# Optimization experiments

Hardware: AMD Instinct MI355X
Metric: run time of the kernel (lower is better)

Reference implementation:

```python
import jax, jax.numpy as jnp
import numpy as np
import math

DIM = 768
HEADS = 12
HEAD_DIM = DIM // HEADS
EPS = 1e-6


def rms_norm(x, w):
    return x * jax.lax.rsqrt(jnp.mean(x * x, axis=-1, keepdims=True) + EPS) * w


def rotate_half(x):
    # torch.cat([-x[..., 1::2], x[..., ::2]], dim=-1)
    return jnp.concatenate([-x[..., 1::2], x[..., ::2]], axis=-1)


def setup_inputs() -> dict:
    key = jax.random.key(0)
    ks = jax.random.split(key, 12)
    b, n = 2, 2048
    s = 0.02
    return {
        "x": jax.random.normal(ks[0], (b, n, DIM), jnp.float32),
        "cos": jax.random.uniform(ks[1], (1, 1, n, HEAD_DIM), jnp.float32),
        "sin": jax.random.uniform(ks[2], (1, 1, n, HEAD_DIM), jnp.float32),
        "mask": jnp.zeros((1, 1, n, n), jnp.float32),
        "wq": jax.random.normal(ks[3], (DIM, DIM), jnp.float32) * s,
        "wk": jax.random.normal(ks[4], (DIM, DIM), jnp.float32) * s,
        "wv": jax.random.normal(ks[5], (DIM, DIM), jnp.float32) * s,
        "wo": jax.random.normal(ks[6], (DIM, DIM), jnp.float32) * s,
        "bo": jnp.zeros((DIM,), jnp.float32),
        "g_attn": jnp.ones((DIM,), jnp.float32),
        "g_ffn": jnp.ones((DIM,), jnp.float32),
        "w1": jax.random.normal(ks[7], (DIM, 4 * DIM), jnp.float32) * s,
        "b1": jnp.zeros((4 * DIM,), jnp.float32),
        "w2": jax.random.normal(ks[8], (4 * DIM, DIM), jnp.float32) * s,
        "b2": jnp.zeros((DIM,), jnp.float32),
    }


def reference(x, cos, sin, mask, wq, wk, wv, wo, bo, g_attn, g_ffn, w1, b1, w2, b2):
    b, n, _ = x.shape
    h = rms_norm(x, g_attn)
    # [b, n, dim] -> [b, heads, n, head_dim]
    def split_heads(t):
        return t.reshape(b, n, HEADS, HEAD_DIM).transpose(0, 2, 1, 3)
    q = split_heads(h @ wq)
    k = split_heads(h @ wk)
    v = split_heads(h @ wv)
    q = q * cos + rotate_half(q) * sin
    k = k * cos + rotate_half(k) * sin
    scores = jnp.einsum("bhqd,bhkd->bhqk", q, k) / math.sqrt(HEAD_DIM)
    scores = scores + mask
    attn = jax.nn.softmax(scores, axis=-1)
    out = jnp.einsum("bhqk,bhkd->bhqd", attn, v)
    out = out.transpose(0, 2, 1, 3).reshape(b, n, DIM)
    x = x + (out @ wo + bo)  # dropout is identity in eval
    h2 = rms_norm(x, g_ffn)
    ffn = jax.nn.silu(h2 @ w1 + b1) @ w2 + b2
    return x + ffn
```

## Files before the change

kernel.cpp:

```cpp
#include <hip/hip_runtime.h>
#include <hip/hip_bf16.h>

typedef unsigned short u16;
typedef unsigned int u32;
typedef float f32x4 __attribute__((ext_vector_type(4)));
typedef short bf16x8 __attribute__((ext_vector_type(8)));
typedef int i32x4 __attribute__((ext_vector_type(4)));
typedef unsigned short u16x8 __attribute__((ext_vector_type(8)));

#define DIM 768
#define NTOK 4096
#define NSEQ 2048
#define NHEAD 12
#define HDIM 64

__device__ __forceinline__ u16 f2bf(float f) {
    u32 u = __builtin_bit_cast(u32, f);
    u32 r = (u + 0x7FFFu + ((u >> 16) & 1u)) >> 16;
    return (u16)r;
}
__device__ __forceinline__ float bf2f(u16 h) {
    return __builtin_bit_cast(float, ((u32)h) << 16);
}

__device__ __forceinline__ void gload16(const void* g, void* l) {
    __builtin_amdgcn_global_load_lds(
        (const __attribute__((address_space(1))) unsigned int*)g,
        (__attribute__((address_space(3))) unsigned int*)l, 16, 0, 0);
}

__global__ __launch_bounds__(256) void rmsnorm_cast(
    const float* __restrict__ X, const float* __restrict__ g, u16* __restrict__ H)
{
    const int row = blockIdx.x;
    const int tid = threadIdx.x;
    const float* xr = X + (long)row * DIM;
    float v0 = xr[tid], v1 = xr[tid + 256], v2 = xr[tid + 512];
    float ss = v0 * v0 + v1 * v1 + v2 * v2;
    #pragma unroll
    for (int o = 1; o < 64; o <<= 1) ss += __shfl_xor(ss, o);
    __shared__ float wsum[4];
    if ((tid & 63) == 0) wsum[tid >> 6] = ss;
    __syncthreads();
    float tot = wsum[0] + wsum[1] + wsum[2] + wsum[3];
    float sc = rsqrtf(tot * (1.0f / DIM) + 1e-6f);
    u16* hr = H + (long)row * DIM;
    hr[tid]       = f2bf(v0 * sc * g[tid]);
    hr[tid + 256] = f2bf(v1 * sc * g[tid + 256]);
    hr[tid + 512] = f2bf(v2 * sc * g[tid + 512]);
}

__device__ __forceinline__ void transpose_cvt_body(
    const float* __restrict__ in, u16* __restrict__ out, int R, int C,
    int bx, int by, int tid)
{
    __shared__ float t[64][65];
    const long ct = (long)bx * 64, rt = (long)by * 64;
    #pragma unroll
    for (int j = 0; j < 4; ++j) {
        int f = j * 256 + tid;
        int row = f >> 4, c0 = (f & 15) * 4;
        f32x4 v = *(const f32x4*)(in + (rt + row) * C + ct + c0);
        #pragma unroll
        for (int i = 0; i < 4; ++i) t[row][c0 + i] = v[i];
    }
    __syncthreads();
    #pragma unroll
    for (int j = 0; j < 2; ++j) {
        int f = j * 256 + tid;
        int c = f >> 3, r0 = (f & 7) * 8;
        u16x8 o;
        #pragma unroll
        for (int i = 0; i < 8; ++i) o[i] = f2bf(t[r0 + i][c]);
        *(u16x8*)(out + (ct + c) * R + rt + r0) = o;
    }
}

__global__ __launch_bounds__(256) void transpose_cvt(
    const float* __restrict__ in, u16* __restrict__ out, int R, int C)
{
    transpose_cvt_body(in, out, R, C, blockIdx.x, blockIdx.y, threadIdx.x);
}

struct Cvt4Args {
    const float* in0; const float* in1; const float* in2; const float* in3;
    u16* out0; u16* out1; u16* out2; u16* out3;
};
__global__ __launch_bounds__(256) void transpose_cvt4(Cvt4Args a)
{
    const float* in; u16* out;
    switch (blockIdx.z) {
        case 0: in = a.in0; out = a.out0; break;
        case 1: in = a.in1; out = a.out1; break;
        case 2: in = a.in2; out = a.out2; break;
        default: in = a.in3; out = a.out3; break;
    }
    transpose_cvt_body(in, out, DIM, DIM, blockIdx.x, blockIdx.y, threadIdx.x);
}

__device__ __forceinline__ void rope_row(const u16* __restrict__ src,
                                         u16* __restrict__ dst,
                                         const float* __restrict__ cs,
                                         const float* __restrict__ sn)
{
    u16x8 qv[8];
    #pragma unroll
    for (int i = 0; i < 8; ++i) qv[i] = ((const u16x8*)src)[i];
    u16x8 ov[8];
    #pragma unroll
    for (int j = 0; j < 32; ++j) {
        float xj  = bf2f(qv[j >> 3][j & 7]);
        float xo  = bf2f(qv[(2 * j + 1) >> 3][(2 * j + 1) & 7]);
        float xhj = bf2f(qv[(32 + j) >> 3][j & 7]);
        float xe  = bf2f(qv[(2 * j) >> 3][(2 * j) & 7]);
        float lo = xj * cs[j] - xo * sn[j];
        float hi = xhj * cs[32 + j] + xe * sn[32 + j];
        ov[j >> 3][j & 7] = f2bf(lo);
        ov[4 + (j >> 3)][j & 7] = f2bf(hi);
    }
    #pragma unroll
    for (int i = 0; i < 8; ++i) ((u16x8*)dst)[i] = ov[i];
}

__global__ __launch_bounds__(256) void rope_qk(
    const u16* __restrict__ QKV, const float* __restrict__ cosT,
    const float* __restrict__ sinT, u16* __restrict__ Qr, u16* __restrict__ Kr)
{
    int gid = blockIdx.x * 256 + threadIdx.x;
    int h = gid % NHEAD, token = gid / NHEAD;
    int b = token >> 11, n = token & 2047;
    const float* cs = cosT + (long)n * HDIM;
    const float* sn = sinT + (long)n * HDIM;
    long dsto = (((long)b * NHEAD + h) * NSEQ + n) * HDIM;
    rope_row(QKV + (long)token * 2304 + h * HDIM,       Qr + dsto, cs, sn);
    rope_row(QKV + (long)token * 2304 + DIM + h * HDIM, Kr + dsto, cs, sn);
}

__global__ __launch_bounds__(256) void v_transpose(
    const u16* __restrict__ QKV, u16* __restrict__ Vt)
{
    __shared__ u32 t[64][65];
    const int tid = threadIdx.x;
    const int nt = blockIdx.x, bh = blockIdx.y;
    const int b = bh / NHEAD, h = bh - b * NHEAD;
    const long tok0 = (long)b * NSEQ + nt * 64;
    #pragma unroll
    for (int j = 0; j < 2; ++j) {
        int f = j * 256 + tid;
        int n = f >> 3, d0 = (f & 7) * 8;
        u16x8 v = *(const u16x8*)(QKV + (tok0 + n) * 2304 + 1536 + h * HDIM + d0);
        #pragma unroll
        for (int i = 0; i < 8; ++i) t[n][d0 + i] = v[i];
    }
    __syncthreads();
    #pragma unroll
    for (int j = 0; j < 2; ++j) {
        int f = j * 256 + tid;
        int d = f >> 3, n0 = (f & 7) * 8;
        u16x8 o;
        #pragma unroll
        for (int i = 0; i < 8; ++i) o[i] = (u16)t[n0 + i][d];
        *(u16x8*)(Vt + ((long)bh * HDIM + d) * NSEQ + nt * 64 + n0) = o;
    }
}

template <int EPI>
__global__ __launch_bounds__(256) void gemm_nt(
    const u16* __restrict__ A, const u16* __restrict__ Bt,
    void* __restrict__ Cp, const float* __restrict__ bias,
    const float* __restrict__ resid, int M, int N, int K, int ldc)
{
    __shared__ __align__(16) char smA[128 * 128];
    __shared__ __align__(16) char smB[128 * 128];
    const int tid = threadIdx.x, lane = tid & 63, wid = tid >> 6;
    const int wr = wid >> 1, wc = wid & 1;
    const long mbase = (long)blockIdx.y * 128, nbase = (long)blockIdx.x * 128;
    const char* Ab = (const char*)A;
    const char* Bb = (const char*)Bt;
    const long strideA = (long)K * 2;

    const f32x4 zero4 = {0.f, 0.f, 0.f, 0.f};
    f32x4 acc[4][4];
    #pragma unroll
    for (int m = 0; m < 4; ++m)
        #pragma unroll
        for (int n = 0; n < 4; ++n) acc[m][n] = zero4;

    const int KT = K >> 6;
    for (int kt = 0; kt < KT; ++kt) {
        const long k0b = (long)kt * 128;
        #pragma unroll
        for (int j = 0; j < 4; ++j) {
            int flat = (j * 256 + tid) * 16;
            int row = flat >> 7, c = flat & 127;
            int csw = c ^ ((row & 7) << 4);
            int ldst = (j * 256 + (tid & 192)) * 16;
            gload16(Ab + (mbase + row) * strideA + k0b + csw, smA + ldst);
            gload16(Bb + (nbase + row) * strideA + k0b + csw, smB + ldst);
        }
        __syncthreads();
        #pragma unroll
        for (int ks = 0; ks < 2; ++ks) {
            const int kbyte = ks * 64 + ((lane >> 4) << 4);
            bf16x8 af[4], bfr[4];
            #pragma unroll
            for (int m = 0; m < 4; ++m) {
                int row = wr * 64 + m * 16 + (lane & 15);
                af[m] = *(const bf16x8*)(smA + row * 128 + (kbyte ^ ((row & 7) << 4)));
            }
            #pragma unroll
            for (int n = 0; n < 4; ++n) {
                int row = wc * 64 + n * 16 + (lane & 15);
                bfr[n] = *(const bf16x8*)(smB + row * 128 + (kbyte ^ ((row & 7) << 4)));
            }
            #pragma unroll
            for (int m = 0; m < 4; ++m)
                #pragma unroll
                for (int n = 0; n < 4; ++n)
                    acc[m][n] = __builtin_amdgcn_mfma_f32_16x16x32_bf16(
                        af[m], bfr[n], acc[m][n], 0, 0, 0);
        }
        __syncthreads();
    }

    #pragma unroll
    for (int m = 0; m < 4; ++m)
        #pragma unroll
        for (int n = 0; n < 4; ++n)
            #pragma unroll
            for (int r = 0; r < 4; ++r) {
                long row = mbase + wr * 64 + m * 16 + ((lane >> 4) << 2) + r;
                long col = nbase + wc * 64 + n * 16 + (lane & 15);
                long idx = row * ldc + col;
                float v = acc[m][n][r];
                if (EPI == 0) {
                    ((u16*)Cp)[idx] = f2bf(v);
                } else if (EPI == 1) {
                    ((float*)Cp)[idx] = resid[idx] + v + bias[col];
                } else {
                    float t = v + bias[col];
                    ((u16*)Cp)[idx] = f2bf(t / (1.0f + __expf(-t)));
                }
            }
}

__global__ __launch_bounds__(256) void attn_fwd(
    const u16* __restrict__ Qr, const u16* __restrict__ Kr,
    const u16* __restrict__ Vt, u16* __restrict__ AO)
{
    __shared__ __align__(16) char smQ[64 * 128];
    __shared__ __align__(16) char smK[64 * 128];
    __shared__ __align__(16) char smV[64 * 128];
    __shared__ __align__(16) char smP[64 * 128];
    const int tid = threadIdx.x, lane = tid & 63, wid = tid >> 6;
    const int qt = blockIdx.x, bh = blockIdx.y;
    const char* Qg = (const char*)(Qr + ((long)bh * NSEQ + qt * 64) * HDIM);
    const char* Kg = (const char*)(Kr + (long)bh * NSEQ * HDIM);
    const char* Vg = (const char*)(Vt + (long)bh * HDIM * NSEQ);

    #pragma unroll
    for (int j = 0; j < 2; ++j) {
        int flat = (j * 256 + tid) * 16;
        int row = flat >> 7, c = flat & 127;
        int csw = c ^ ((row & 7) << 4);
        gload16(Qg + row * 128 + csw, smQ + (j * 256 + (tid & 192)) * 16);
    }
    __syncthreads();
    bf16x8 qf[2];
    #pragma unroll
    for (int ks = 0; ks < 2; ++ks) {
        int row = wid * 16 + (lane & 15);
        int kbyte = ks * 64 + ((lane >> 4) << 4);
        qf[ks] = *(const bf16x8*)(smQ + row * 128 + (kbyte ^ ((row & 7) << 4)));
    }

    const f32x4 zero4 = {0.f, 0.f, 0.f, 0.f};
    f32x4 oacc[4];
    float mst[4], lst[4];
    #pragma unroll
    for (int df = 0; df < 4; ++df) oacc[df] = zero4;
    #pragma unroll
    for (int r = 0; r < 4; ++r) { mst[r] = -1e30f; lst[r] = 0.f; }

    for (int kb = 0; kb < 32; ++kb) {
        #pragma unroll
        for (int j = 0; j < 2; ++j) {
            int flat = (j * 256 + tid) * 16;
            int row = flat >> 7, c = flat & 127;
            int csw = c ^ ((row & 7) << 4);
            int ldst = (j * 256 + (tid & 192)) * 16;
            gload16(Kg + ((long)kb * 64 + row) * 128 + csw, smK + ldst);
            gload16(Vg + (long)row * (NSEQ * 2) + kb * 128 + csw, smV + ldst);
        }
        __syncthreads();

        f32x4 s[4];
        #pragma unroll
        for (int n = 0; n < 4; ++n) s[n] = zero4;
        #pragma unroll
        for (int ks = 0; ks < 2; ++ks) {
            int kbyte = ks * 64 + ((lane >> 4) << 4);
            bf16x8 kf[4];
            #pragma unroll
            for (int n = 0; n < 4; ++n) {
                int row = n * 16 + (lane & 15);
                kf[n] = *(const bf16x8*)(smK + row * 128 + (kbyte ^ ((row & 7) << 4)));
            }
            #pragma unroll
            for (int n = 0; n < 4; ++n)
                s[n] = __builtin_amdgcn_mfma_f32_16x16x32_bf16(
                    qf[ks], kf[n], s[n], 0, 0, 0);
        }

        float rmax[4] = {-1e30f, -1e30f, -1e30f, -1e30f};
        #pragma unroll
        for (int n = 0; n < 4; ++n)
            #pragma unroll
            for (int r = 0; r < 4; ++r) {
                s[n][r] *= 0.125f;
                rmax[r] = fmaxf(rmax[r], s[n][r]);
            }
        #pragma unroll
        for (int o = 1; o < 16; o <<= 1)
            #pragma unroll
            for (int r = 0; r < 4; ++r)
                rmax[r] = fmaxf(rmax[r], __shfl_xor(rmax[r], o));
        float corr[4], rsum[4] = {0.f, 0.f, 0.f, 0.f};
        #pragma unroll
        for (int r = 0; r < 4; ++r) {
            float mnew = fmaxf(mst[r], rmax[r]);
            corr[r] = __expf(mst[r] - mnew);
            mst[r] = mnew;
        }
        #pragma unroll
        for (int n = 0; n < 4; ++n)
            #pragma unroll
            for (int r = 0; r < 4; ++r) {
                float p = __expf(s[n][r] - mst[r]);
                s[n][r] = p;
                rsum[r] += p;
            }
        #pragma unroll
        for (int o = 1; o < 16; o <<= 1)
            #pragma unroll
            for (int r = 0; r < 4; ++r) rsum[r] += __shfl_xor(rsum[r], o);
        #pragma unroll
        for (int r = 0; r < 4; ++r) lst[r] = lst[r] * corr[r] + rsum[r];
        #pragma unroll
        for (int df = 0; df < 4; ++df)
            #pragma unroll
            for (int r = 0; r < 4; ++r) oacc[df][r] *= corr[r];
        #pragma unroll
        for (int n = 0; n < 4; ++n)
            #pragma unroll
            for (int r = 0; r < 4; ++r) {
                int row = wid * 16 + ((lane >> 4) << 2) + r;
                int colb = (n * 16 + (lane & 15)) * 2;
                *(u16*)(smP + row * 128 + (colb ^ ((row & 7) << 4))) = f2bf(s[n][r]);
            }

        #pragma unroll
        for (int ks = 0; ks < 2; ++ks) {
            int kbyte = ks * 64 + ((lane >> 4) << 4);
            bf16x8 vf[4];
            #pragma unroll
            for (int df = 0; df < 4; ++df) {
                int row = df * 16 + (lane & 15);
                vf[df] = *(const bf16x8*)(smV + row * 128 + (kbyte ^ ((row & 7) << 4)));
            }
            int rowp = wid * 16 + (lane & 15);
            bf16x8 pf = *(const bf16x8*)(smP + rowp * 128 + (kbyte ^ ((rowp & 7) << 4)));
            #pragma unroll
            for (int df = 0; df < 4; ++df)
                oacc[df] = __builtin_amdgcn_mfma_f32_16x16x32_bf16(
                    pf, vf[df], oacc[df], 0, 0, 0);
        }
        __syncthreads();
    }

    const int b = bh / NHEAD, h = bh - b * NHEAD;
    #pragma unroll
    for (int df = 0; df < 4; ++df)
        #pragma unroll
        for (int r = 0; r < 4; ++r) {
            long token = (long)b * NSEQ + qt * 64 + wid * 16 + ((lane >> 4) << 2) + r;
            int col = h * HDIM + df * 16 + (lane & 15);
            AO[token * DIM + col] = f2bf(oacc[df][r] / lst[r]);
        }
}

extern "C" void kernel_launch(void* const* d_in, const int* in_sizes, int n_in,
                              void* d_out, int out_size, void* d_ws, size_t ws_size,
                              hipStream_t stream) {
    const float* x      = (const float*)d_in[0];
    const float* cosT   = (const float*)d_in[1];
    const float* sinT   = (const float*)d_in[2];
    const float* wq     = (const float*)d_in[4];
    const float* wk     = (const float*)d_in[5];
    const float* wv     = (const float*)d_in[6];
    const float* wo     = (const float*)d_in[7];
    const float* bo     = (const float*)d_in[8];
    const float* g_attn = (const float*)d_in[9];
    const float* g_ffn  = (const float*)d_in[10];
    const float* w1     = (const float*)d_in[11];
    const float* b1     = (const float*)d_in[12];
    const float* w2     = (const float*)d_in[13];
    const float* b2     = (const float*)d_in[14];
    float* out = (float*)d_out;
    char* ws = (char*)d_ws;

    constexpr long SZ_H    = (long)NTOK * DIM * 2;
    constexpr long SZ_WQKV = 2304L * DIM * 2;
    constexpr long SZ_WO   = (long)DIM * DIM * 2;
    constexpr long SZ_W1   = 3072L * DIM * 2;
    constexpr long SZ_W2   = (long)DIM * 3072 * 2;
    constexpr long SZ_QKV  = (long)NTOK * 2304 * 2;
    constexpr long SZ_QR   = 24L * NSEQ * HDIM * 2;
    constexpr long SZ_AO   = (long)NTOK * DIM * 2;

    const long OFF_H    = 0;
    const long OFF_WQKV = OFF_H + SZ_H;
    const long OFF_WO   = OFF_WQKV + SZ_WQKV;
    const long OFF_W1   = OFF_WO + SZ_WO;
    const long OFF_W2   = OFF_W1 + SZ_W1;
    const long OFF_QKV  = OFF_W2 + SZ_W2;
    const long OFF_QR   = OFF_QKV + SZ_QKV;
    const long OFF_KR   = OFF_QR + SZ_QR;
    const long OFF_VT   = OFF_KR + SZ_QR;
    const long OFF_AO   = OFF_VT + SZ_QR;
    const long OFF_X2   = OFF_AO + SZ_AO;
    const long OFF_FFN1 = OFF_QKV;

    u16* H     = (u16*)(ws + OFF_H);
    u16* WQKVT = (u16*)(ws + OFF_WQKV);
    u16* WOT   = (u16*)(ws + OFF_WO);
    u16* W1T   = (u16*)(ws + OFF_W1);
    u16* W2T   = (u16*)(ws + OFF_W2);
    u16* QKV   = (u16*)(ws + OFF_QKV);
    u16* QR    = (u16*)(ws + OFF_QR);
    u16* KR    = (u16*)(ws + OFF_KR);
    u16* VT    = (u16*)(ws + OFF_VT);
    u16* AO    = (u16*)(ws + OFF_AO);
    float* X2  = (float*)(ws + OFF_X2);
    u16* FFN1  = (u16*)(ws + OFF_FFN1);

    Cvt4Args c4 = { wq, wk, wv, wo,
                    WQKVT, WQKVT + 768L * 768, WQKVT + 2L * 768 * 768, WOT };
    transpose_cvt4<<<dim3(12, 12, 4), 256, 0, stream>>>(c4);
    transpose_cvt<<<dim3(48, 12), 256, 0, stream>>>(w1, W1T, DIM, 3072);
    transpose_cvt<<<dim3(12, 48), 256, 0, stream>>>(w2, W2T, 3072, DIM);

    rmsnorm_cast<<<NTOK, 256, 0, stream>>>(x, g_attn, H);
    gemm_nt<0><<<dim3(18, 32), 256, 0, stream>>>(H, WQKVT, QKV, nullptr, nullptr,
                                                 NTOK, 2304, DIM, 2304);
    rope_qk<<<192, 256, 0, stream>>>(QKV, cosT, sinT, QR, KR);
    v_transpose<<<dim3(32, 24), 256, 0, stream>>>(QKV, VT);
    attn_fwd<<<dim3(32, 24), 256, 0, stream>>>(QR, KR, VT, AO);
    gemm_nt<1><<<dim3(6, 32), 256, 0, stream>>>(AO, WOT, X2, bo, x,
                                                NTOK, DIM, DIM, DIM);

    rmsnorm_cast<<<NTOK, 256, 0, stream>>>(X2, g_ffn, H);
    gemm_nt<2><<<dim3(24, 32), 256, 0, stream>>>(H, W1T, FFN1, b1, nullptr,
                                                 NTOK, 3072, DIM, 3072);
    gemm_nt<1><<<dim3(6, 32), 256, 0, stream>>>(FFN1, W2T, out, b2, X2,
                                                NTOK, DIM, 3072, DIM);
}
```

Measured before the change: 372.5 us.

## Double-buffer GEMM and attention tiles, lazy softmax rescale, smaller M tiles

Adds double-buffered LDS staging to the GEMM and attention kernels, so the next K tile (or K/V block) is fetched while the current one is being computed, and drops the barrier that followed each load. Attention now skips the online-softmax rescale of the accumulators unless the running max grows by more than 8, and remaps block indices so blocks sharing a head run close together for better L2 reuse. The N=768 GEMMs use 64-row M tiles, which doubles their block count to fill more compute units. The cost is twice the LDS per block, which may reduce occupancy, and correctness relies on the end-of-loop barrier also waiting for the asynchronous loads.

```diff
diff --git a/kernel.cpp b/kernel.cpp
--- a/kernel.cpp
+++ b/kernel.cpp
@@ -164,57 +164,71 @@
     }
 }
 
-template <int EPI>
+template <int EPI, int MF>
 __global__ __launch_bounds__(256) void gemm_nt(
     const u16* __restrict__ A, const u16* __restrict__ Bt,
     void* __restrict__ Cp, const float* __restrict__ bias,
     const float* __restrict__ resid, int M, int N, int K, int ldc)
 {
-    __shared__ __align__(16) char smA[128 * 128];
-    __shared__ __align__(16) char smB[128 * 128];
+    constexpr int BM = MF * 32;
+    __shared__ __align__(16) char smA[2][BM * 128];
+    __shared__ __align__(16) char smB[2][128 * 128];
     const int tid = threadIdx.x, lane = tid & 63, wid = tid >> 6;
     const int wr = wid >> 1, wc = wid & 1;
-    const long mbase = (long)blockIdx.y * 128, nbase = (long)blockIdx.x * 128;
+    const long mbase = (long)blockIdx.y * BM, nbase = (long)blockIdx.x * 128;
     const char* Ab = (const char*)A;
     const char* Bb = (const char*)Bt;
     const long strideA = (long)K * 2;
 
-    const f32x4 zero4 = {0.f, 0.f, 0.f, 0.f};
-    f32x4 acc[4][4];
-    #pragma unroll
-    for (int m = 0; m < 4; ++m)
-        #pragma unroll
-        for (int n = 0; n < 4; ++n) acc[m][n] = zero4;
-
-    const int KT = K >> 6;
-    for (int kt = 0; kt < KT; ++kt) {
+    auto stage = [&](int buf, int kt) {
         const long k0b = (long)kt * 128;
+        #pragma unroll
+        for (int j = 0; j < MF; ++j) {
+            int flat = (j * 256 + tid) * 16;
+            int row = flat >> 7, c = flat & 127;
+            int csw = c ^ ((row & 7) << 4);
+            gload16(Ab + (mbase + row) * strideA + k0b + csw,
+                    smA[buf] + (j * 256 + (tid & 192)) * 16);
+        }
         #pragma unroll
         for (int j = 0; j < 4; ++j) {
             int flat = (j * 256 + tid) * 16;
             int row = flat >> 7, c = flat & 127;
             int csw = c ^ ((row & 7) << 4);
-            int ldst = (j * 256 + (tid & 192)) * 16;
-            gload16(Ab + (mbase + row) * strideA + k0b + csw, smA + ldst);
-            gload16(Bb + (nbase + row) * strideA + k0b + csw, smB + ldst);
-        }
-        __syncthreads();
+            gload16(Bb + (nbase + row) * strideA + k0b + csw,
+                    smB[buf] + (j * 256 + (tid & 192)) * 16);
+        }
+    };
+
+    const f32x4 zero4 = {0.f, 0.f, 0.f, 0.f};
+    f32x4 acc[MF][4];
+    #pragma unroll
+    for (int m = 0; m < MF; ++m)
+        #pragma unroll
+        for (int n = 0; n < 4; ++n) acc[m][n] = zero4;
+
+    const int KT = K >> 6;
+    stage(0, 0);
+    __syncthreads();
+    for (int kt = 0; kt < KT; ++kt) {
+        const int cur = kt & 1;
+        if (kt + 1 < KT) stage(cur ^ 1, kt + 1);
         #pragma unroll
         for (int ks = 0; ks < 2; ++ks) {
             const int kbyte = ks * 64 + ((lane >> 4) << 4);
-            bf16x8 af[4], bfr[4];
-            #pragma unroll
-            for (int m = 0; m < 4; ++m) {
-                int row = wr * 64 + m * 16 + (lane & 15);
-                af[m] = *(const bf16x8*)(smA + row * 128 + (kbyte ^ ((row & 7) << 4)));
+            bf16x8 af[MF], bfr[4];
+            #pragma unroll
+            for (int m = 0; m < MF; ++m) {
+                int row = wr * (MF * 16) + m * 16 + (lane & 15);
+                af[m] = *(const bf16x8*)(smA[cur] + row * 128 + (kbyte ^ ((row & 7) << 4)));
             }
             #pragma unroll
             for (int n = 0; n < 4; ++n) {
                 int row = wc * 64 + n * 16 + (lane & 15);
-                bfr[n] = *(const bf16x8*)(smB + row * 128 + (kbyte ^ ((row & 7) << 4)));
-            }
-            #pragma unroll
-            for (int m = 0; m < 4; ++m)
+                bfr[n] = *(const bf16x8*)(smB[cur] + row * 128 + (kbyte ^ ((row & 7) << 4)));
+            }
+            #pragma unroll
+            for (int m = 0; m < MF; ++m)
                 #pragma unroll
                 for (int n = 0; n < 4; ++n)
                     acc[m][n] = __builtin_amdgcn_mfma_f32_16x16x32_bf16(
@@ -224,12 +238,12 @@
     }
 
     #pragma unroll
-    for (int m = 0; m < 4; ++m)
+    for (int m = 0; m < MF; ++m)
         #pragma unroll
         for (int n = 0; n < 4; ++n)
             #pragma unroll
             for (int r = 0; r < 4; ++r) {
-                long row = mbase + wr * 64 + m * 16 + ((lane >> 4) << 2) + r;
+                long row = mbase + wr * (MF * 16) + m * 16 + ((lane >> 4) << 2) + r;
                 long col = nbase + wc * 64 + n * 16 + (lane & 15);
                 long idx = row * ldc + col;
                 float v = acc[m][n][r];
@@ -249,14 +263,27 @@
     const u16* __restrict__ Vt, u16* __restrict__ AO)
 {
     __shared__ __align__(16) char smQ[64 * 128];
-    __shared__ __align__(16) char smK[64 * 128];
-    __shared__ __align__(16) char smV[64 * 128];
+    __shared__ __align__(16) char smK[2][64 * 128];
+    __shared__ __align__(16) char smV[2][64 * 128];
     __shared__ __align__(16) char smP[64 * 128];
     const int tid = threadIdx.x, lane = tid & 63, wid = tid >> 6;
-    const int qt = blockIdx.x, bh = blockIdx.y;
+    const int i = blockIdx.x;
+    const int bh = 8 * (i >> 8) + (i & 7), qt = (i & 255) >> 3;
     const char* Qg = (const char*)(Qr + ((long)bh * NSEQ + qt * 64) * HDIM);
     const char* Kg = (const char*)(Kr + (long)bh * NSEQ * HDIM);
     const char* Vg = (const char*)(Vt + (long)bh * HDIM * NSEQ);
+
+    auto stageKV = [&](int buf, int kb) {
+        #pragma unroll
+        for (int j = 0; j < 2; ++j) {
+            int flat = (j * 256 + tid) * 16;
+            int row = flat >> 7, c = flat & 127;
+            int csw = c ^ ((row & 7) << 4);
+            int ldst = (j * 256 + (tid & 192)) * 16;
+            gload16(Kg + ((long)kb * 64 + row) * 128 + csw, smK[buf] + ldst);
+            gload16(Vg + (long)row * (NSEQ * 2) + kb * 128 + csw, smV[buf] + ldst);
+        }
+    };
 
     #pragma unroll
     for (int j = 0; j < 2; ++j) {
@@ -265,7 +292,9 @@
         int csw = c ^ ((row & 7) << 4);
         gload16(Qg + row * 128 + csw, smQ + (j * 256 + (tid & 192)) * 16);
     }
+    stageKV(0, 0);
     __syncthreads();
+
     bf16x8 qf[2];
     #pragma unroll
     for (int ks = 0; ks < 2; ++ks) {
@@ -283,16 +312,8 @@
     for (int r = 0; r < 4; ++r) { mst[r] = -1e30f; lst[r] = 0.f; }
 
     for (int kb = 0; kb < 32; ++kb) {
-        #pragma unroll
-        for (int j = 0; j < 2; ++j) {
-            int flat = (j * 256 + tid) * 16;
-            int row = flat >> 7, c = flat & 127;
-            int csw = c ^ ((row & 7) << 4);
-            int ldst = (j * 256 + (tid & 192)) * 16;
-            gload16(Kg + ((long)kb * 64 + row) * 128 + csw, smK + ldst);
-            gload16(Vg + (long)row * (NSEQ * 2) + kb * 128 + csw, smV + ldst);
-        }
-        __syncthreads();
+        const int cur = kb & 1;
+        if (kb + 1 < 32) stageKV(cur ^ 1, kb + 1);
 
         f32x4 s[4];
         #pragma unroll
@@ -304,7 +325,7 @@
             #pragma unroll
             for (int n = 0; n < 4; ++n) {
                 int row = n * 16 + (lane & 15);
-                kf[n] = *(const bf16x8*)(smK + row * 128 + (kbyte ^ ((row & 7) << 4)));
+                kf[n] = *(const bf16x8*)(smK[cur] + row * 128 + (kbyte ^ ((row & 7) << 4)));
             }
             #pragma unroll
             for (int n = 0; n < 4; ++n)
@@ -325,13 +346,21 @@
             #pragma unroll
             for (int r = 0; r < 4; ++r)
                 rmax[r] = fmaxf(rmax[r], __shfl_xor(rmax[r], o));
-        float corr[4], rsum[4] = {0.f, 0.f, 0.f, 0.f};
-        #pragma unroll
-        for (int r = 0; r < 4; ++r) {
-            float mnew = fmaxf(mst[r], rmax[r]);
-            corr[r] = __expf(mst[r] - mnew);
-            mst[r] = mnew;
-        }
+        float growth = rmax[0] - mst[0];
+        #pragma unroll
+        for (int r = 1; r < 4; ++r) growth = fmaxf(growth, rmax[r] - mst[r]);
+        if (growth > 8.0f) {
+            #pragma unroll
+            for (int r = 0; r < 4; ++r) {
+                float mnew = fmaxf(mst[r], rmax[r]);
+                float corr = __expf(mst[r] - mnew);
+                mst[r] = mnew;
+                lst[r] *= corr;
+                #pragma unroll
+                for (int df = 0; df < 4; ++df) oacc[df][r] *= corr;
+            }
+        }
+        float rsum[4] = {0.f, 0.f, 0.f, 0.f};
         #pragma unroll
         for (int n = 0; n < 4; ++n)
             #pragma unroll
@@ -345,11 +374,7 @@
             #pragma unroll
             for (int r = 0; r < 4; ++r) rsum[r] += __shfl_xor(rsum[r], o);
         #pragma unroll
-        for (int r = 0; r < 4; ++r) lst[r] = lst[r] * corr[r] + rsum[r];
-        #pragma unroll
-        for (int df = 0; df < 4; ++df)
-            #pragma unroll
-            for (int r = 0; r < 4; ++r) oacc[df][r] *= corr[r];
+        for (int r = 0; r < 4; ++r) lst[r] += rsum[r];
         #pragma unroll
         for (int n = 0; n < 4; ++n)
             #pragma unroll
@@ -366,7 +391,7 @@
             #pragma unroll
             for (int df = 0; df < 4; ++df) {
                 int row = df * 16 + (lane & 15);
-                vf[df] = *(const bf16x8*)(smV + row * 128 + (kbyte ^ ((row & 7) << 4)));
+                vf[df] = *(const bf16x8*)(smV[cur] + row * 128 + (kbyte ^ ((row & 7) << 4)));
             }
             int rowp = wid * 16 + (lane & 15);
             bf16x8 pf = *(const bf16x8*)(smP + rowp * 128 + (kbyte ^ ((rowp & 7) << 4)));
@@ -451,17 +476,17 @@
     transpose_cvt<<<dim3(12, 48), 256, 0, stream>>>(w2, W2T, 3072, DIM);
 
     rmsnorm_cast<<<NTOK, 256, 0, stream>>>(x, g_attn, H);
-    gemm_nt<0><<<dim3(18, 32), 256, 0, stream>>>(H, WQKVT, QKV, nullptr, nullptr,
-                                                 NTOK, 2304, DIM, 2304);
+    gemm_nt<0, 4><<<dim3(18, 32), 256, 0, stream>>>(H, WQKVT, QKV, nullptr, nullptr,
+                                                    NTOK, 2304, DIM, 2304);
     rope_qk<<<192, 256, 0, stream>>>(QKV, cosT, sinT, QR, KR);
     v_transpose<<<dim3(32, 24), 256, 0, stream>>>(QKV, VT);
-    attn_fwd<<<dim3(32, 24), 256, 0, stream>>>(QR, KR, VT, AO);
-    gemm_nt<1><<<dim3(6, 32), 256, 0, stream>>>(AO, WOT, X2, bo, x,
-                                                NTOK, DIM, DIM, DIM);
+    attn_fwd<<<768, 256, 0, stream>>>(QR, KR, VT, AO);
+    gemm_nt<1, 2><<<dim3(6, 64), 256, 0, stream>>>(AO, WOT, X2, bo, x,
+                                                   NTOK, DIM, DIM, DIM);
 
     rmsnorm_cast<<<NTOK, 256, 0, stream>>>(X2, g_ffn, H);
-    gemm_nt<2><<<dim3(24, 32), 256, 0, stream>>>(H, W1T, FFN1, b1, nullptr,
-                                                 NTOK, 3072, DIM, 3072);
-    gemm_nt<1><<<dim3(6, 32), 256, 0, stream>>>(FFN1, W2T, out, b2, X2,
-                                                NTOK, DIM, 3072, DIM);
-}
+    gemm_nt<2, 4><<<dim3(24, 32), 256, 0, stream>>>(H, W1T, FFN1, b1, nullptr,
+                                                    NTOK, 3072, DIM, 3072);
+    gemm_nt<1, 2><<<dim3(6, 64), 256, 0, stream>>>(FFN1, W2T, out, b2, X2,
+                                                   NTOK, DIM, 3072, DIM);
+}
```

New measurement: 347.3 us. -6.8%, faster.
